# Kernel tuning notes

Measured on AMD Instinct MI355X. Metric: run time of the kernel, lower is better.

Reference implementation:

```python
import jax, jax.numpy as jnp
import numpy as np

NH, DK, DV = 8, 10, 10  # num_heads, per-head key dim, per-head value dim (dim_k=dim_v=80)


def setup_inputs() -> dict:
    key = jax.random.key(0)
    k1, k2, k3, k4, k5 = jax.random.split(key, 5)
    B, NX, NY = 64, 512, 512
    x = jax.random.normal(k1, (B, NX, 768), dtype=jnp.float32)
    y = jax.random.normal(k2, (B, NY, 283), dtype=jnp.float32)
    # nn.Linear(bias=False) weights, stored transposed as (in, out); scaled init
    Wq = jax.random.normal(k3, (768, 80), dtype=jnp.float32) * 0.02
    Wk = jax.random.normal(k4, (283, 80), dtype=jnp.float32) * 0.02
    Wv = jax.random.normal(k5, (283, 80), dtype=jnp.float32) * 0.02
    return {"x": x, "y": y, "Wq": Wq, "Wk": Wk, "Wv": Wv}


def reference(x, y, Wq, Wk, Wv):
    B, nx, _ = x.shape
    ny = y.shape[1]
    # projections -> split heads: (B, nh, seq, dhead)
    q = (x @ Wq).reshape(B, nx, NH, DK).transpose(0, 2, 1, 3)
    k = (y @ Wk).reshape(B, ny, NH, DK).transpose(0, 2, 1, 3)
    v = (y @ Wv).reshape(B, ny, NH, DV).transpose(0, 2, 1, 3)
    scale = 1.0 / np.sqrt(DK).astype(np.float32)
    dist = jax.nn.softmax(jnp.einsum("bhqd,bhkd->bhqk", q, k) * scale, axis=-1)
    att = q + jnp.einsum("bhqk,bhkd->bhqd", dist, v)  # residual add of q
    att = att.transpose(0, 2, 1, 3).reshape(B, nx, NH * DV)
    # module returns `result` = flattened attention (fc/BN stack is dead code)
    return att.reshape(B, -1)
```

## Files before the change

kernel.cpp:

```cpp
#include <hip/hip_runtime.h>
#include <stdint.h>

typedef unsigned short u16;
typedef unsigned int   u32;
typedef _Float16       f16;

typedef __attribute__((ext_vector_type(2))) _Float16 half2v;
typedef __attribute__((ext_vector_type(4))) _Float16 half4v;
typedef __attribute__((ext_vector_type(8))) _Float16 half8v;
typedef __attribute__((ext_vector_type(4))) float    floatx4;

#define NXS    512
#define NYS    512
#define NHEAD  8
#define DHEAD  10
#define DMODEL 80
#define DXK    768
#define DYK    283
#define DYKP   288

__device__ inline half2v pk2(float x, float y) {
  return __builtin_bit_cast(half2v, __builtin_amdgcn_cvt_pkrtz(x, y));
}
__device__ inline half4v cvt4(float4 v) {
  return __builtin_shufflevector(pk2(v.x, v.y), pk2(v.z, v.w), 0, 1, 2, 3);
}
__device__ inline half8v cvt8(float4 a, float4 b) {
  const half4v lo = cvt4(a), hi = cvt4(b);
  return __builtin_shufflevector(lo, hi, 0, 1, 2, 3, 4, 5, 6, 7);
}
__device__ inline half4v h4u32(u32 a, u32 b) {
  return __builtin_shufflevector(__builtin_bit_cast(half2v, a),
                                 __builtin_bit_cast(half2v, b), 0, 1, 2, 3);
}

__global__ __launch_bounds__(256) void w_prep(const float* __restrict__ Wq,
                                              const float* __restrict__ Wk,
                                              const float* __restrict__ Wv,
                                              f16* __restrict__ Tq,
                                              f16* __restrict__ Tk,
                                              f16* __restrict__ Tv) {
  const int idx = blockIdx.x * 256 + threadIdx.x;
  if (idx < 80 * 768) {
    const int c = idx / 768, k = idx - c * 768;
    Tq[idx] = (f16)Wq[k * 80 + c];
  }
  if (idx < 80 * 288) {
    const int c = idx / 288, k = idx - c * 288;
    float a = 0.f, b = 0.f;
    if (k < DYK) { a = Wk[k * 80 + c]; b = Wv[k * 80 + c]; }
    Tk[idx] = (f16)a;
    Tv[idx] = (f16)b;
  }
}

__global__ __launch_bounds__(256, 4) void proj(const float* __restrict__ X,
                                               const float* __restrict__ Y,
                                               const f16* __restrict__ Wtq,
                                               const f16* __restrict__ Wtk,
                                               const f16* __restrict__ Wtv,
                                               f16* __restrict__ Qw,
                                               f16* __restrict__ Kw,
                                               f16* __restrict__ Vw) {
  const int t = threadIdx.x;
  const int wv = t >> 6, lane = t & 63, m16 = lane & 15, quad = lane >> 4;
  const int blk = blockIdx.x;
  const int tile = blk >> 1;
  const int row0 = tile * 64;
  const int row = row0 + wv * 16 + m16;
  const int kq = quad * 8;

  if (!(blk & 1)) {
    const float* xrow = X + (size_t)row * DXK + kq;
    const f16*   wqb  = Wtq + m16 * DXK + kq;

    floatx4 acc[5];
#pragma unroll
    for (int i = 0; i < 5; ++i) acc[i] = (floatx4){0.f, 0.f, 0.f, 0.f};

#pragma unroll
    for (int s = 0; s < 24; ++s) {
      const float4 xa = *(const float4*)(xrow + s * 32);
      const float4 xb = *(const float4*)(xrow + s * 32 + 4);
      const half8v a = cvt8(xa, xb);
#pragma unroll
      for (int nt = 0; nt < 5; ++nt) {
        const half8v b = *(const half8v*)(wqb + nt * 16 * DXK + s * 32);
        acc[nt] = __builtin_amdgcn_mfma_f32_16x16x32_f16(a, b, acc[nt], 0, 0, 0);
      }
    }

#pragma unroll
    for (int nt = 0; nt < 5; ++nt) {
      const int col = nt * 16 + m16;
#pragma unroll
      for (int p = 0; p < 4; ++p) {
        const int grow = row0 + wv * 16 + quad * 4 + p;
        Qw[(size_t)grow * DMODEL + col] = (f16)acc[nt][p];
      }
    }
  } else {
    const float* yrow = Y + (size_t)row * DYK;
    const f16*   wkb  = Wtk + m16 * DYKP + kq;
    const f16*   wvb  = Wtv + m16 * DYKP + kq;

    floatx4 ak[5], av[5];
#pragma unroll
    for (int i = 0; i < 5; ++i) {
      ak[i] = (floatx4){0.f, 0.f, 0.f, 0.f};
      av[i] = (floatx4){0.f, 0.f, 0.f, 0.f};
    }

#pragma unroll
    for (int s = 0; s < 9; ++s) {
      const int k0 = s * 32 + kq;
      float yr[8];
#pragma unroll
      for (int j = 0; j < 8; ++j)
        yr[j] = (k0 + j < DYK) ? yrow[k0 + j] : 0.f;
      half8v a;
#pragma unroll
      for (int j = 0; j < 8; ++j) a[j] = (f16)yr[j];
#pragma unroll
      for (int nt = 0; nt < 5; ++nt) {
        const half8v bk = *(const half8v*)(wkb + nt * 16 * DYKP + s * 32);
        ak[nt] = __builtin_amdgcn_mfma_f32_16x16x32_f16(a, bk, ak[nt], 0, 0, 0);
        const half8v bv = *(const half8v*)(wvb + nt * 16 * DYKP + s * 32);
        av[nt] = __builtin_amdgcn_mfma_f32_16x16x32_f16(a, bv, av[nt], 0, 0, 0);
      }
    }

#pragma unroll
    for (int nt = 0; nt < 5; ++nt) {
      const int col = nt * 16 + m16;
      const int h = col / 10, d = col - h * 10;
#pragma unroll
      for (int p = 0; p < 4; ++p) {
        const int grow = row0 + wv * 16 + quad * 4 + p;
        const int bb = grow >> 9, ny = grow & 511;
        const size_t o = (((size_t)bb * NHEAD + h) * NYS + ny) * DHEAD + d;
        Kw[o] = (f16)ak[nt][p];
        Vw[o] = (f16)av[nt][p];
      }
    }
  }
}

__global__ __launch_bounds__(256) void attn(const f16* __restrict__ Q,
                                            const f16* __restrict__ K,
                                            const f16* __restrict__ V,
                                            float* __restrict__ O) {
  __shared__ f16 Ks[512 * 22];
  __shared__ f16 Vt[16 * 522];
  const int t = threadIdx.x;
  const int wv = t >> 6, lane = t & 63, m16 = lane & 15, quad = lane >> 4;
  const int bh = blockIdx.x >> 1, half = blockIdx.x & 1;
  const int b = bh >> 3, h = bh & 7;

  const u32* Kg = (const u32*)K + (size_t)bh * NYS * 5;
  const u32* Vg = (const u32*)V + (size_t)bh * NYS * 5;
  for (int idx = t; idx < 2560; idx += 256) {
    const u32 row = (u32)idx / 5u, c = (u32)idx - row * 5u;
    const half2v kv = __builtin_bit_cast(half2v, Kg[idx]);
    Ks[row * 22 + 2 * c]     = kv[0];
    Ks[row * 22 + 2 * c + 1] = kv[1];
    const half2v vvv = __builtin_bit_cast(half2v, Vg[idx]);
    Vt[(2 * c) * 522 + row]     = vvv[0];
    Vt[(2 * c + 1) * 522 + row] = vvv[1];
  }
  for (int idx = t; idx < 3072; idx += 256) {
    const u32 row = (u32)idx / 6u, d = 10u + ((u32)idx - row * 6u);
    Ks[row * 22 + d] = (f16)0.f;
  }
  for (int idx = t; idx < 6 * 522; idx += 256)
    Vt[10 * 522 + idx] = (f16)0.f;
  __syncthreads();

  const float scale = 0.31622776601683794f;
#pragma unroll 1
  for (int i = 0; i < 4; ++i) {
    const int qt = half * 16 + wv * 4 + i;
    const int qrow = qt * 16 + m16;
    const u32* Qg32 = (const u32*)(Q + ((size_t)b * NXS + qrow) * DMODEL + h * DHEAD);
    float s0 = 0.f, s1 = 0.f, s2 = 0.f, s3 = 0.f;
    if (quad < 2) {
      const u32 ua = Qg32[quad * 2], ub = Qg32[quad * 2 + 1];
      const half2v ha = __builtin_bit_cast(half2v, ua);
      const half2v hb = __builtin_bit_cast(half2v, ub);
      s0 = (float)ha[0]; s1 = (float)ha[1]; s2 = (float)hb[0]; s3 = (float)hb[1];
    } else if (quad == 2) {
      const u32 ua = Qg32[4];
      const half2v ha = __builtin_bit_cast(half2v, ua);
      s0 = (float)ha[0]; s1 = (float)ha[1];
    }
    const half4v qf = __builtin_shufflevector(pk2(s0 * scale, s1 * scale),
                                              pk2(s2 * scale, s3 * scale),
                                              0, 1, 2, 3);
    floatx4 o0 = (floatx4){0.f, 0.f, 0.f, 0.f};
    floatx4 o1 = (floatx4){0.f, 0.f, 0.f, 0.f};
    float l0 = 0.f, l1 = 0.f;
    for (int kt = 0; kt < 32; kt += 2) {
#pragma unroll
      for (int u = 0; u < 2; ++u) {
        const int ktu = kt + u;
        const int kb = (ktu * 16 + m16) * 22 + quad * 4;
        const half4v kf = h4u32(*(const u32*)&Ks[kb], *(const u32*)&Ks[kb + 2]);
        const floatx4 s = __builtin_amdgcn_mfma_f32_16x16x16f16(
            kf, qf, (floatx4){0.f, 0.f, 0.f, 0.f}, 0, 0, 0);
        const float p0 = __expf(s[0]);
        const float p1 = __expf(s[1]);
        const float p2 = __expf(s[2]);
        const float p3 = __expf(s[3]);
        const half4v pf = __builtin_shufflevector(pk2(p0, p1), pk2(p2, p3),
                                                  0, 1, 2, 3);
        const int vb = m16 * 522 + ktu * 16 + quad * 4;
        const half4v vf = h4u32(*(const u32*)&Vt[vb], *(const u32*)&Vt[vb + 2]);
        if (u == 0) {
          l0 += (p0 + p1) + (p2 + p3);
          o0 = __builtin_amdgcn_mfma_f32_16x16x16f16(pf, vf, o0, 0, 0, 0);
        } else {
          l1 += (p0 + p1) + (p2 + p3);
          o1 = __builtin_amdgcn_mfma_f32_16x16x16f16(pf, vf, o1, 0, 0, 0);
        }
      }
    }
    float lp = l0 + l1;
    lp += __shfl_xor(lp, 16);
    lp += __shfl_xor(lp, 32);
#pragma unroll
    for (int p = 0; p < 4; ++p) {
      const int rq = qt * 16 + quad * 4 + p;
      const float lr = __shfl(lp, quad * 4 + p);
      if (m16 < DHEAD) {
        const float qres = (float)Q[((size_t)b * NXS + rq) * DMODEL + h * DHEAD + m16];
        O[((size_t)b * NXS + rq) * DMODEL + h * DHEAD + m16] =
            qres + (o0[p] + o1[p]) / lr;
      }
    }
  }
}

extern "C" void kernel_launch(void* const* d_in, const int* in_sizes, int n_in,
                              void* d_out, int out_size, void* d_ws, size_t ws_size,
                              hipStream_t stream) {
  const float* x  = (const float*)d_in[0];
  const float* y  = (const float*)d_in[1];
  const float* Wq = (const float*)d_in[2];
  const float* Wk = (const float*)d_in[3];
  const float* Wv = (const float*)d_in[4];
  float* out = (float*)d_out;

  char* ws = (char*)d_ws;
  f16* Wtq = (f16*)(ws);
  f16* Wtk = (f16*)(ws + 122880);
  f16* Wtv = (f16*)(ws + 168960);
  f16* Qw  = (f16*)(ws + 262144);
  f16* Kw  = (f16*)(ws + 5505024);
  f16* Vw  = (f16*)(ws + 10747904);

  w_prep<<<240, 256, 0, stream>>>(Wq, Wk, Wv, Wtq, Wtk, Wtv);
  proj  <<<1024, 256, 0, stream>>>(x, y, Wtq, Wtk, Wtv, Qw, Kw, Vw);
  attn  <<<1024, 256, 0, stream>>>(Qw, Kw, Vw, out);
}
```

Measured before the change: 280.4 us.

## Stage projection tiles through LDS with register-prefetched double buffering

The projection kernel now loads X/Y and weight tiles cooperatively with coalesced wide loads, converts them to fp16, and stages them in padded shared memory. MFMA operands are then read from LDS, while the next k-chunk is prefetched into registers. Before this, each lane gathered its operands straight from global memory with strided per-row reads. The weight prep kernel is rewritten to read coalesced and write transposed, and the K/V padding grows to 320 to fit 64-wide chunks. The cost is extra barriers, more LDS and register pressure, and possible occupancy loss.

```diff
diff --git a/kernel.cpp b/kernel.cpp
--- a/kernel.cpp
+++ b/kernel.cpp
@@ -17,17 +17,13 @@
 #define DMODEL 80
 #define DXK    768
 #define DYK    283
-#define DYKP   288
+#define DYKP   320
 
 __device__ inline half2v pk2(float x, float y) {
   return __builtin_bit_cast(half2v, __builtin_amdgcn_cvt_pkrtz(x, y));
 }
 __device__ inline half4v cvt4(float4 v) {
   return __builtin_shufflevector(pk2(v.x, v.y), pk2(v.z, v.w), 0, 1, 2, 3);
-}
-__device__ inline half8v cvt8(float4 a, float4 b) {
-  const half4v lo = cvt4(a), hi = cvt4(b);
-  return __builtin_shufflevector(lo, hi, 0, 1, 2, 3, 4, 5, 6, 7);
 }
 __device__ inline half4v h4u32(u32 a, u32 b) {
   return __builtin_shufflevector(__builtin_bit_cast(half2v, a),
@@ -40,17 +36,20 @@
                                               f16* __restrict__ Tq,
                                               f16* __restrict__ Tk,
                                               f16* __restrict__ Tv) {
-  const int idx = blockIdx.x * 256 + threadIdx.x;
-  if (idx < 80 * 768) {
-    const int c = idx / 768, k = idx - c * 768;
-    Tq[idx] = (f16)Wq[k * 80 + c];
-  }
-  if (idx < 80 * 288) {
-    const int c = idx / 288, k = idx - c * 288;
-    float a = 0.f, b = 0.f;
-    if (k < DYK) { a = Wk[k * 80 + c]; b = Wv[k * 80 + c]; }
-    Tk[idx] = (f16)a;
-    Tv[idx] = (f16)b;
+  const int i = blockIdx.x * 256 + threadIdx.x;
+  if (i < 768 * 80) {
+    const int k = i / 80, c = i - k * 80;
+    Tq[c * DXK + k] = (f16)Wq[i];
+  }
+  if (i < 283 * 80) {
+    const int k = i / 80, c = i - k * 80;
+    Tk[c * DYKP + k] = (f16)Wk[i];
+    Tv[c * DYKP + k] = (f16)Wv[i];
+  }
+  if (i < 80 * 37) {
+    const int c = i / 37, k = DYK + (i - c * 37);
+    Tk[c * DYKP + k] = (f16)0.f;
+    Tv[c * DYKP + k] = (f16)0.f;
   }
 }
 
@@ -62,32 +61,94 @@
                                                f16* __restrict__ Qw,
                                                f16* __restrict__ Kw,
                                                f16* __restrict__ Vw) {
+  __shared__ f16 smem[64 * 72 + 2 * 80 * 72];
   const int t = threadIdx.x;
   const int wv = t >> 6, lane = t & 63, m16 = lane & 15, quad = lane >> 4;
   const int blk = blockIdx.x;
-  const int tile = blk >> 1;
-  const int row0 = tile * 64;
-  const int row = row0 + wv * 16 + m16;
-  const int kq = quad * 8;
+  const int row0 = (blk >> 1) * 64;
+  const int u0 = t, u1 = t + 256, u2 = t + 512;
 
   if (!(blk & 1)) {
-    const float* xrow = X + (size_t)row * DXK + kq;
-    const f16*   wqb  = Wtq + m16 * DXK + kq;
+    f16* Xs = smem;
+    f16* Ws = smem + 64 * 72;
+    const float* Xb = X + (size_t)row0 * DXK;
+
+    float4 xb0[4], xb1[4];
+    uint4 wb0, wb1, wb2;
+#pragma unroll
+    for (int i = 0; i < 4; ++i) {
+      const int vi = t + 256 * i;
+      xb0[i] = *(const float4*)&Xb[(vi >> 4) * DXK + (vi & 15) * 4];
+    }
+#pragma unroll
+    for (int i = 0; i < 4; ++i) {
+      const int vi = t + 256 * i;
+      xb1[i] = *(const float4*)&Xb[(vi >> 4) * DXK + 64 + (vi & 15) * 4];
+    }
+    wb0 = *(const uint4*)&Wtq[(u0 >> 3) * DXK + (u0 & 7) * 8];
+    wb1 = *(const uint4*)&Wtq[(u1 >> 3) * DXK + (u1 & 7) * 8];
+    if (t < 128) wb2 = *(const uint4*)&Wtq[(u2 >> 3) * DXK + (u2 & 7) * 8];
 
     floatx4 acc[5];
 #pragma unroll
     for (int i = 0; i < 5; ++i) acc[i] = (floatx4){0.f, 0.f, 0.f, 0.f};
 
-#pragma unroll
-    for (int s = 0; s < 24; ++s) {
-      const float4 xa = *(const float4*)(xrow + s * 32);
-      const float4 xb = *(const float4*)(xrow + s * 32 + 4);
-      const half8v a = cvt8(xa, xb);
-#pragma unroll
-      for (int nt = 0; nt < 5; ++nt) {
-        const half8v b = *(const half8v*)(wqb + nt * 16 * DXK + s * 32);
-        acc[nt] = __builtin_amdgcn_mfma_f32_16x16x32_f16(a, b, acc[nt], 0, 0, 0);
-      }
+#define Q_STORE_LDS(XB)                                                        \
+    do {                                                                       \
+      _Pragma("unroll")                                                        \
+      for (int i = 0; i < 4; ++i) {                                            \
+        const int vi = t + 256 * i;                                            \
+        *(half4v*)&Xs[(vi >> 4) * 72 + (vi & 15) * 4] = cvt4(XB[i]);           \
+      }                                                                        \
+      *(uint4*)&Ws[(u0 >> 3) * 72 + (u0 & 7) * 8] = wb0;                       \
+      *(uint4*)&Ws[(u1 >> 3) * 72 + (u1 & 7) * 8] = wb1;                       \
+      if (t < 128) *(uint4*)&Ws[(u2 >> 3) * 72 + (u2 & 7) * 8] = wb2;          \
+    } while (0)
+
+#define Q_LOAD_X(XB, S)                                                        \
+    do {                                                                       \
+      const int k0_ = (S) * 64;                                                \
+      _Pragma("unroll")                                                        \
+      for (int i = 0; i < 4; ++i) {                                            \
+        const int vi = t + 256 * i;                                            \
+        XB[i] = *(const float4*)&Xb[(vi >> 4) * DXK + k0_ + (vi & 15) * 4];    \
+      }                                                                        \
+    } while (0)
+
+#define Q_LOAD_W(S)                                                            \
+    do {                                                                       \
+      const int k0_ = (S) * 64;                                                \
+      wb0 = *(const uint4*)&Wtq[(u0 >> 3) * DXK + k0_ + (u0 & 7) * 8];         \
+      wb1 = *(const uint4*)&Wtq[(u1 >> 3) * DXK + k0_ + (u1 & 7) * 8];         \
+      if (t < 128) wb2 = *(const uint4*)&Wtq[(u2 >> 3) * DXK + k0_ + (u2 & 7) * 8]; \
+    } while (0)
+
+#define Q_COMPUTE()                                                            \
+    do {                                                                       \
+      _Pragma("unroll")                                                        \
+      for (int kk = 0; kk < 2; ++kk) {                                         \
+        const half8v a = *(const half8v*)&Xs[(wv * 16 + m16) * 72 + kk * 32 + quad * 8]; \
+        _Pragma("unroll")                                                      \
+        for (int nt = 0; nt < 5; ++nt) {                                       \
+          const half8v b = *(const half8v*)&Ws[(nt * 16 + m16) * 72 + kk * 32 + quad * 8]; \
+          acc[nt] = __builtin_amdgcn_mfma_f32_16x16x32_f16(a, b, acc[nt], 0, 0, 0); \
+        }                                                                      \
+      }                                                                        \
+    } while (0)
+
+    for (int s = 0; s < 12; s += 2) {
+      if (s) __syncthreads();
+      Q_STORE_LDS(xb0);
+      __syncthreads();
+      if (s + 2 < 12) Q_LOAD_X(xb0, s + 2);
+      Q_LOAD_W(s + 1);
+      Q_COMPUTE();
+      __syncthreads();
+      Q_STORE_LDS(xb1);
+      __syncthreads();
+      if (s + 3 < 12) Q_LOAD_X(xb1, s + 3);
+      if (s + 2 < 12) Q_LOAD_W(s + 2);
+      Q_COMPUTE();
     }
 
 #pragma unroll
@@ -100,9 +161,41 @@
       }
     }
   } else {
-    const float* yrow = Y + (size_t)row * DYK;
-    const f16*   wkb  = Wtk + m16 * DYKP + kq;
-    const f16*   wvb  = Wtv + m16 * DYKP + kq;
+    f16* Ys  = smem;
+    f16* Wks = smem + 64 * 72;
+    f16* Wvs = smem + 64 * 72 + 80 * 72;
+    const float* Yb = Y + (size_t)row0 * DYK;
+
+    float yb[2][16];
+    uint4 wk0, wk1, wk2, wvr0, wvr1, wvr2;
+
+#define KV_LOAD_Y(BI, S)                                                       \
+    do {                                                                       \
+      _Pragma("unroll")                                                        \
+      for (int i = 0; i < 16; ++i) {                                           \
+        const int idx = t + 256 * i;                                           \
+        const int r = idx >> 6, kk = idx & 63;                                 \
+        const int k = (S) * 64 + kk;                                           \
+        yb[BI][i] = (k < DYK) ? Yb[(size_t)r * DYK + k] : 0.f;                 \
+      }                                                                        \
+    } while (0)
+
+#define KV_LOAD_W(S)                                                           \
+    do {                                                                       \
+      const int k0_ = (S) * 64;                                                \
+      wk0 = *(const uint4*)&Wtk[(u0 >> 3) * DYKP + k0_ + (u0 & 7) * 8];        \
+      wk1 = *(const uint4*)&Wtk[(u1 >> 3) * DYKP + k0_ + (u1 & 7) * 8];        \
+      wvr0 = *(const uint4*)&Wtv[(u0 >> 3) * DYKP + k0_ + (u0 & 7) * 8];       \
+      wvr1 = *(const uint4*)&Wtv[(u1 >> 3) * DYKP + k0_ + (u1 & 7) * 8];       \
+      if (t < 128) {                                                           \
+        wk2  = *(const uint4*)&Wtk[(u2 >> 3) * DYKP + k0_ + (u2 & 7) * 8];     \
+        wvr2 = *(const uint4*)&Wtv[(u2 >> 3) * DYKP + k0_ + (u2 & 7) * 8];     \
+      }                                                                        \
+    } while (0)
+
+    KV_LOAD_Y(0, 0);
+    KV_LOAD_Y(1, 1);
+    KV_LOAD_W(0);
 
     floatx4 ak[5], av[5];
 #pragma unroll
@@ -112,21 +205,34 @@
     }
 
 #pragma unroll
-    for (int s = 0; s < 9; ++s) {
-      const int k0 = s * 32 + kq;
-      float yr[8];
-#pragma unroll
-      for (int j = 0; j < 8; ++j)
-        yr[j] = (k0 + j < DYK) ? yrow[k0 + j] : 0.f;
-      half8v a;
-#pragma unroll
-      for (int j = 0; j < 8; ++j) a[j] = (f16)yr[j];
-#pragma unroll
-      for (int nt = 0; nt < 5; ++nt) {
-        const half8v bk = *(const half8v*)(wkb + nt * 16 * DYKP + s * 32);
-        ak[nt] = __builtin_amdgcn_mfma_f32_16x16x32_f16(a, bk, ak[nt], 0, 0, 0);
-        const half8v bv = *(const half8v*)(wvb + nt * 16 * DYKP + s * 32);
-        av[nt] = __builtin_amdgcn_mfma_f32_16x16x32_f16(a, bv, av[nt], 0, 0, 0);
+    for (int s = 0; s < 5; ++s) {
+      if (s) __syncthreads();
+#pragma unroll
+      for (int i = 0; i < 16; ++i) {
+        const int idx = t + 256 * i;
+        Ys[(idx >> 6) * 72 + (idx & 63)] = (f16)yb[s & 1][i];
+      }
+      *(uint4*)&Wks[(u0 >> 3) * 72 + (u0 & 7) * 8] = wk0;
+      *(uint4*)&Wks[(u1 >> 3) * 72 + (u1 & 7) * 8] = wk1;
+      *(uint4*)&Wvs[(u0 >> 3) * 72 + (u0 & 7) * 8] = wvr0;
+      *(uint4*)&Wvs[(u1 >> 3) * 72 + (u1 & 7) * 8] = wvr1;
+      if (t < 128) {
+        *(uint4*)&Wks[(u2 >> 3) * 72 + (u2 & 7) * 8] = wk2;
+        *(uint4*)&Wvs[(u2 >> 3) * 72 + (u2 & 7) * 8] = wvr2;
+      }
+      __syncthreads();
+      if (s + 2 < 5) KV_LOAD_Y(s & 1, s + 2);
+      if (s + 1 < 5) KV_LOAD_W(s + 1);
+#pragma unroll
+      for (int kk = 0; kk < 2; ++kk) {
+        const half8v a = *(const half8v*)&Ys[(wv * 16 + m16) * 72 + kk * 32 + quad * 8];
+#pragma unroll
+        for (int nt = 0; nt < 5; ++nt) {
+          const half8v bk = *(const half8v*)&Wks[(nt * 16 + m16) * 72 + kk * 32 + quad * 8];
+          ak[nt] = __builtin_amdgcn_mfma_f32_16x16x32_f16(a, bk, ak[nt], 0, 0, 0);
+          const half8v bv = *(const half8v*)&Wvs[(nt * 16 + m16) * 72 + kk * 32 + quad * 8];
+          av[nt] = __builtin_amdgcn_mfma_f32_16x16x32_f16(a, bv, av[nt], 0, 0, 0);
+        }
       }
     }
 
@@ -253,7 +359,7 @@
   char* ws = (char*)d_ws;
   f16* Wtq = (f16*)(ws);
   f16* Wtk = (f16*)(ws + 122880);
-  f16* Wtv = (f16*)(ws + 168960);
+  f16* Wtv = (f16*)(ws + 174080);
   f16* Qw  = (f16*)(ws + 262144);
   f16* Kw  = (f16*)(ws + 5505024);
   f16* Vw  = (f16*)(ws + 10747904);
```

Result: faster. 274.6 us (-2.1%).

## Stage projection tiles through double-buffered LDS with coalesced loads

Applied to the files above, without the earlier changes.

Rewrites the projection kernel so X/Y and weight tiles are loaded with coalesced row-wise global reads, converted to f16 and staged into double-buffered shared memory, and MFMA operands are read from LDS. Block indexing now puts all Q blocks first, then K/V blocks, instead of interleaving them. The aim is better global memory coalescing (the old per-lane strided Y reads were poorly coalesced) and overlapping loads with MFMA. In exchange it adds LDS traffic, barriers and about 35KB of shared memory per block, which may reduce occupancy.

```diff
diff --git a/kernel.cpp b/kernel.cpp
--- a/kernel.cpp
+++ b/kernel.cpp
@@ -24,10 +24,6 @@
 }
 __device__ inline half4v cvt4(float4 v) {
   return __builtin_shufflevector(pk2(v.x, v.y), pk2(v.z, v.w), 0, 1, 2, 3);
-}
-__device__ inline half8v cvt8(float4 a, float4 b) {
-  const half4v lo = cvt4(a), hi = cvt4(b);
-  return __builtin_shufflevector(lo, hi, 0, 1, 2, 3, 4, 5, 6, 7);
 }
 __device__ inline half4v h4u32(u32 a, u32 b) {
   return __builtin_shufflevector(__builtin_bit_cast(half2v, a),
@@ -62,32 +58,74 @@
                                                f16* __restrict__ Qw,
                                                f16* __restrict__ Kw,
                                                f16* __restrict__ Vw) {
+  __shared__ f16 smem[2 * 8960];
   const int t = threadIdx.x;
   const int wv = t >> 6, lane = t & 63, m16 = lane & 15, quad = lane >> 4;
   const int blk = blockIdx.x;
-  const int tile = blk >> 1;
-  const int row0 = tile * 64;
-  const int row = row0 + wv * 16 + m16;
-  const int kq = quad * 8;
-
-  if (!(blk & 1)) {
-    const float* xrow = X + (size_t)row * DXK + kq;
-    const f16*   wqb  = Wtq + m16 * DXK + kq;
+
+  if (blk < 512) {
+    const int row0 = blk * 64;
+    const int xr_r = t >> 3, xr_k = (t & 7) << 2;
+    const int wi0 = t, wi1 = t + 160;
+    f16* const bufQ0 = smem;
+    f16* const bufQ1 = smem + 8960;
+
+    float4 xa0, xa1, xb0, xb1;
+    uint4 wa0, wa1, wb0, wb1;
+
+#define Q_LOAD(X0, X1, W0, W1, S)                                              \
+    do {                                                                       \
+      const int k0_ = (S) * 32;                                                \
+      X0 = *(const float4*)&X[(size_t)(row0 + xr_r) * DXK + k0_ + xr_k];       \
+      X1 = *(const float4*)&X[(size_t)(row0 + xr_r + 32) * DXK + k0_ + xr_k];  \
+      if (t < 160) {                                                           \
+        W0 = *(const uint4*)&Wtq[(wi0 >> 2) * DXK + k0_ + (wi0 & 3) * 8];      \
+        W1 = *(const uint4*)&Wtq[(wi1 >> 2) * DXK + k0_ + (wi1 & 3) * 8];      \
+      }                                                                        \
+    } while (0)
+
+#define Q_STORE(BUF, X0, X1, W0, W1)                                           \
+    do {                                                                       \
+      f16* const Xs_ = (BUF);                                                  \
+      f16* const Ws_ = (BUF) + 2560;                                           \
+      *(half4v*)&Xs_[xr_r * 40 + xr_k] = cvt4(X0);                             \
+      *(half4v*)&Xs_[(xr_r + 32) * 40 + xr_k] = cvt4(X1);                      \
+      if (t < 160) {                                                           \
+        *(uint4*)&Ws_[(wi0 >> 2) * 40 + (wi0 & 3) * 8] = W0;                   \
+        *(uint4*)&Ws_[(wi1 >> 2) * 40 + (wi1 & 3) * 8] = W1;                   \
+      }                                                                        \
+    } while (0)
+
+#define Q_COMPUTE(BUF)                                                         \
+    do {                                                                       \
+      f16* const Xs_ = (BUF);                                                  \
+      f16* const Ws_ = (BUF) + 2560;                                           \
+      const half8v a = *(const half8v*)&Xs_[(wv * 16 + m16) * 40 + quad * 8];  \
+      _Pragma("unroll")                                                        \
+      for (int nt = 0; nt < 5; ++nt) {                                         \
+        const half8v b = *(const half8v*)&Ws_[(nt * 16 + m16) * 40 + quad * 8];\
+        acc[nt] = __builtin_amdgcn_mfma_f32_16x16x32_f16(a, b, acc[nt], 0, 0, 0); \
+      }                                                                        \
+    } while (0)
 
     floatx4 acc[5];
 #pragma unroll
     for (int i = 0; i < 5; ++i) acc[i] = (floatx4){0.f, 0.f, 0.f, 0.f};
 
-#pragma unroll
-    for (int s = 0; s < 24; ++s) {
-      const float4 xa = *(const float4*)(xrow + s * 32);
-      const float4 xb = *(const float4*)(xrow + s * 32 + 4);
-      const half8v a = cvt8(xa, xb);
-#pragma unroll
-      for (int nt = 0; nt < 5; ++nt) {
-        const half8v b = *(const half8v*)(wqb + nt * 16 * DXK + s * 32);
-        acc[nt] = __builtin_amdgcn_mfma_f32_16x16x32_f16(a, b, acc[nt], 0, 0, 0);
-      }
+    Q_LOAD(xa0, xa1, wa0, wa1, 0);
+    Q_LOAD(xb0, xb1, wb0, wb1, 1);
+    Q_STORE(bufQ0, xa0, xa1, wa0, wa1);
+    __syncthreads();
+
+    for (int s = 0; s < 24; s += 2) {
+      Q_COMPUTE(bufQ0);
+      if (s + 2 < 24) Q_LOAD(xa0, xa1, wa0, wa1, s + 2);
+      Q_STORE(bufQ1, xb0, xb1, wb0, wb1);
+      __syncthreads();
+      Q_COMPUTE(bufQ1);
+      if (s + 3 < 24) Q_LOAD(xb0, xb1, wb0, wb1, s + 3);
+      if (s + 2 < 24) Q_STORE(bufQ0, xa0, xa1, wa0, wa1);
+      __syncthreads();
     }
 
 #pragma unroll
@@ -100,9 +138,63 @@
       }
     }
   } else {
-    const float* yrow = Y + (size_t)row * DYK;
-    const f16*   wkb  = Wtk + m16 * DYKP + kq;
-    const f16*   wvb  = Wtv + m16 * DYKP + kq;
+    const int row0 = (blk - 512) * 64;
+    const int wi0 = t, wi1 = t + 160;
+    f16* const bufK0 = smem;
+    f16* const bufK1 = smem + 8960;
+
+    float ya[8], yb[8];
+    uint4 wka0, wka1, wva0, wva1, wkb0, wkb1, wvb0, wvb1;
+
+#define KV_LOAD(YR, WK0, WK1, WV0, WV1, S)                                     \
+    do {                                                                       \
+      const int k0_ = (S) * 32;                                                \
+      _Pragma("unroll")                                                        \
+      for (int i = 0; i < 8; ++i) {                                            \
+        const int idx = t + 256 * i;                                           \
+        const int r = idx >> 5, k = k0_ + (idx & 31);                          \
+        YR[i] = (k < DYK) ? Y[(size_t)(row0 + r) * DYK + k] : 0.f;             \
+      }                                                                        \
+      if (t < 160) {                                                           \
+        WK0 = *(const uint4*)&Wtk[(wi0 >> 2) * DYKP + k0_ + (wi0 & 3) * 8];    \
+        WK1 = *(const uint4*)&Wtk[(wi1 >> 2) * DYKP + k0_ + (wi1 & 3) * 8];    \
+        WV0 = *(const uint4*)&Wtv[(wi0 >> 2) * DYKP + k0_ + (wi0 & 3) * 8];    \
+        WV1 = *(const uint4*)&Wtv[(wi1 >> 2) * DYKP + k0_ + (wi1 & 3) * 8];    \
+      }                                                                        \
+    } while (0)
+
+#define KV_STORE(BUF, YR, WK0, WK1, WV0, WV1)                                  \
+    do {                                                                       \
+      f16* const Ys_  = (BUF);                                                 \
+      f16* const Wks_ = (BUF) + 2560;                                          \
+      f16* const Wvs_ = (BUF) + 5760;                                          \
+      _Pragma("unroll")                                                        \
+      for (int i = 0; i < 8; ++i) {                                            \
+        const int idx = t + 256 * i;                                           \
+        Ys_[(idx >> 5) * 40 + (idx & 31)] = (f16)YR[i];                        \
+      }                                                                        \
+      if (t < 160) {                                                           \
+        *(uint4*)&Wks_[(wi0 >> 2) * 40 + (wi0 & 3) * 8] = WK0;                 \
+        *(uint4*)&Wks_[(wi1 >> 2) * 40 + (wi1 & 3) * 8] = WK1;                 \
+        *(uint4*)&Wvs_[(wi0 >> 2) * 40 + (wi0 & 3) * 8] = WV0;                 \
+        *(uint4*)&Wvs_[(wi1 >> 2) * 40 + (wi1 & 3) * 8] = WV1;                 \
+      }                                                                        \
+    } while (0)
+
+#define KV_COMPUTE(BUF)                                                        \
+    do {                                                                       \
+      f16* const Ys_  = (BUF);                                                 \
+      f16* const Wks_ = (BUF) + 2560;                                          \
+      f16* const Wvs_ = (BUF) + 5760;                                          \
+      const half8v a = *(const half8v*)&Ys_[(wv * 16 + m16) * 40 + quad * 8];  \
+      _Pragma("unroll")                                                        \
+      for (int nt = 0; nt < 5; ++nt) {                                         \
+        const half8v bk = *(const half8v*)&Wks_[(nt * 16 + m16) * 40 + quad * 8]; \
+        ak[nt] = __builtin_amdgcn_mfma_f32_16x16x32_f16(a, bk, ak[nt], 0, 0, 0); \
+        const half8v bv = *(const half8v*)&Wvs_[(nt * 16 + m16) * 40 + quad * 8]; \
+        av[nt] = __builtin_amdgcn_mfma_f32_16x16x32_f16(a, bv, av[nt], 0, 0, 0); \
+      }                                                                        \
+    } while (0)
 
     floatx4 ak[5], av[5];
 #pragma unroll
@@ -111,24 +203,22 @@
       av[i] = (floatx4){0.f, 0.f, 0.f, 0.f};
     }
 
-#pragma unroll
-    for (int s = 0; s < 9; ++s) {
-      const int k0 = s * 32 + kq;
-      float yr[8];
-#pragma unroll
-      for (int j = 0; j < 8; ++j)
-        yr[j] = (k0 + j < DYK) ? yrow[k0 + j] : 0.f;
-      half8v a;
-#pragma unroll
-      for (int j = 0; j < 8; ++j) a[j] = (f16)yr[j];
-#pragma unroll
-      for (int nt = 0; nt < 5; ++nt) {
-        const half8v bk = *(const half8v*)(wkb + nt * 16 * DYKP + s * 32);
-        ak[nt] = __builtin_amdgcn_mfma_f32_16x16x32_f16(a, bk, ak[nt], 0, 0, 0);
-        const half8v bv = *(const half8v*)(wvb + nt * 16 * DYKP + s * 32);
-        av[nt] = __builtin_amdgcn_mfma_f32_16x16x32_f16(a, bv, av[nt], 0, 0, 0);
-      }
-    }
+    KV_LOAD(ya, wka0, wka1, wva0, wva1, 0);
+    KV_LOAD(yb, wkb0, wkb1, wvb0, wvb1, 1);
+    KV_STORE(bufK0, ya, wka0, wka1, wva0, wva1);
+    __syncthreads();
+
+    for (int s = 0; s < 8; s += 2) {
+      KV_COMPUTE(bufK0);
+      if (s + 2 < 9) KV_LOAD(ya, wka0, wka1, wva0, wva1, s + 2);
+      KV_STORE(bufK1, yb, wkb0, wkb1, wvb0, wvb1);
+      __syncthreads();
+      KV_COMPUTE(bufK1);
+      if (s + 3 < 9) KV_LOAD(yb, wkb0, wkb1, wvb0, wvb1, s + 3);
+      if (s + 2 < 9) KV_STORE(bufK0, ya, wka0, wka1, wva0, wva1);
+      __syncthreads();
+    }
+    KV_COMPUTE(bufK0);
 
 #pragma unroll
     for (int nt = 0; nt < 5; ++nt) {
```

New measurement: 250.1 us. 10.8% less time.
